# Kernel optimization log

Hardware: AMD Instinct MI355X
Metric: run time of the kernel (lower is better)

## Reference

```python
import jax, jax.numpy as jnp
import numpy as np

FLOAT_MIN = -100000.0

def setup_inputs() -> dict:
    key = jax.random.key(0)
    ks = jax.random.split(key, 6)
    B, S, Q, K = 16, 8192, 1024, 256
    stdv = 1.0 / np.sqrt(K)
    return {
        "query": jax.random.normal(ks[0], (B, Q), dtype=jnp.float32),
        "keys": jax.random.normal(ks[1], (B, S, K), dtype=jnp.float32),
        "values": jax.random.normal(ks[2], (B, S, K), dtype=jnp.float32),
        "kv_mask": jnp.ones((B, S, 1), dtype=jnp.float32),
        "W_attr": jax.random.uniform(ks[3], (K, Q), jnp.float32, -stdv, stdv),
        "b_attr": jax.random.uniform(ks[4], (K,), jnp.float32, -stdv, stdv),
        "V_attr": jax.random.uniform(ks[5], (K,), jnp.float32, -stdv, stdv),
    }

def reference(query, keys, values, kv_mask, W_attr, b_attr, V_attr):
    # projected query: [B, 1, K]
    q = jnp.einsum('bq,kq->bk', query, W_attr)[:, None, :]
    # additive energies: [B, S, 1]
    energies = jnp.einsum('bsk,k->bs', jnp.tanh(keys + q + b_attr), V_attr)[:, :, None]
    energies = kv_mask * energies + (1.0 - kv_mask) * FLOAT_MIN
    scores = jax.nn.softmax(energies, axis=1)          # [B, S, 1]
    ctx = jnp.sum(values * scores, axis=1)             # [B, V_dim]
    return (scores, ctx)
```

## Files before the change

kernel.cpp:

```cpp
#include <hip/hip_runtime.h>
#include <math.h>

#define BB 16
#define SS 8192
#define KK 256
#define QQ 1024

static constexpr float C2L2E = 2.88539008177792681f;
static constexpr float FLOAT_MIN_V = -100000.0f;

__device__ __forceinline__ float wave_sum(float v) {
#pragma unroll
  for (int off = 32; off >= 1; off >>= 1) v += __shfl_xor(v, off, 64);
  return v;
}

__global__ __launch_bounds__(256) void qproj_kernel(
    const float* __restrict__ query, const float* __restrict__ W,
    const float* __restrict__ b_attr, float* __restrict__ qb2) {
  const int blk = blockIdx.x;
  const int b = blk >> 6;
  const int kg = blk & 63;
  const int lane = threadIdx.x & 63;
  const int w = threadIdx.x >> 6;
  const int k = kg * 4 + w;

  const float4* q4 = (const float4*)(query + (size_t)b * QQ);
  const float4* w4 = (const float4*)(W + (size_t)k * QQ);
  float acc = 0.f;
#pragma unroll
  for (int j = 0; j < 4; ++j) {
    const float4 qv = q4[j * 64 + lane];
    const float4 wv = w4[j * 64 + lane];
    acc = fmaf(wv.x, qv.x, acc);
    acc = fmaf(wv.y, qv.y, acc);
    acc = fmaf(wv.z, qv.z, acc);
    acc = fmaf(wv.w, qv.w, acc);
  }
  acc = wave_sum(acc);
  if (lane == 0) qb2[b * KK + k] = C2L2E * (acc + b_attr[k]);
}

#define EROWS 64
__global__ __launch_bounds__(256) void energy_kernel(
    const float* __restrict__ keys, const float* __restrict__ V_attr,
    const float* __restrict__ qb2, float* __restrict__ e) {
  const int blk = blockIdx.x;
  const int b = blk / (SS / EROWS);
  const int lane = threadIdx.x & 63;
  const int w = threadIdx.x >> 6;
  const int s0 = (blk % (SS / EROWS)) * EROWS + w * (EROWS / 4);

  const float4 v4 = ((const float4*)V_attr)[lane];
  const float sv = wave_sum(v4.x + v4.y + v4.z + v4.w);
  const float4 nv2 =
      make_float4(-2.f * v4.x, -2.f * v4.y, -2.f * v4.z, -2.f * v4.w);
  const float4 qb = ((const float4*)qb2)[b * (KK / 4) + lane];

  const float* rowbase = keys + (size_t)(b * SS + s0) * KK;
  float4 kv = ((const float4*)rowbase)[lane];
  for (int i = 0; i < EROWS / 4; ++i) {
    const float4 cur = kv;
    if (i < EROWS / 4 - 1)
      kv = ((const float4*)(rowbase + (size_t)(i + 1) * KK))[lane];
    float r0 = __builtin_amdgcn_rcpf(
        1.f + __builtin_amdgcn_exp2f(fmaf(cur.x, C2L2E, qb.x)));
    float r1 = __builtin_amdgcn_rcpf(
        1.f + __builtin_amdgcn_exp2f(fmaf(cur.y, C2L2E, qb.y)));
    float r2 = __builtin_amdgcn_rcpf(
        1.f + __builtin_amdgcn_exp2f(fmaf(cur.z, C2L2E, qb.z)));
    float r3 = __builtin_amdgcn_rcpf(
        1.f + __builtin_amdgcn_exp2f(fmaf(cur.w, C2L2E, qb.w)));
    float p = fmaf(nv2.x, r0,
                   fmaf(nv2.y, r1, fmaf(nv2.z, r2, nv2.w * r3)));
    p = wave_sum(p);
    if (lane == 0) e[b * SS + s0 + i] = p + sv;
  }
}

__global__ __launch_bounds__(1024) void softmax_kernel(
    const float* __restrict__ e, const float* __restrict__ mask,
    float* __restrict__ scores) {
  const int b = blockIdx.x;
  const int tid = threadIdx.x;
  const int lane = tid & 63;
  const int wid = tid >> 6;
  __shared__ float red[16];

  float ev[8];
  float m = -3.4e38f;
#pragma unroll
  for (int i = 0; i < 8; ++i) {
    const int s = tid + i * 1024;
    const float mk = mask[b * SS + s];
    float x = e[b * SS + s];
    x = mk * x + (1.f - mk) * FLOAT_MIN_V;
    ev[i] = x;
    m = fmaxf(m, x);
  }
#pragma unroll
  for (int off = 32; off >= 1; off >>= 1) m = fmaxf(m, __shfl_xor(m, off, 64));
  if (lane == 0) red[wid] = m;
  __syncthreads();
  if (wid == 0) {
    float t = red[lane & 15];
#pragma unroll
    for (int off = 8; off >= 1; off >>= 1) t = fmaxf(t, __shfl_xor(t, off, 64));
    if (lane == 0) red[0] = t;
  }
  __syncthreads();
  m = red[0];
  __syncthreads();

  float pv[8];
  float l = 0.f;
#pragma unroll
  for (int i = 0; i < 8; ++i) {
    pv[i] = __expf(ev[i] - m);
    l += pv[i];
  }
  l = wave_sum(l);
  if (lane == 0) red[wid] = l;
  __syncthreads();
  if (wid == 0) {
    float t = red[lane & 15];
#pragma unroll
    for (int off = 8; off >= 1; off >>= 1) t += __shfl_xor(t, off, 64);
    if (lane == 0) red[0] = t;
  }
  __syncthreads();
  const float inv = 1.f / red[0];
#pragma unroll
  for (int i = 0; i < 8; ++i) scores[b * SS + tid + i * 1024] = pv[i] * inv;
}

#define CROWS 64
__global__ __launch_bounds__(256) void ctx_partial_kernel(
    const float* __restrict__ values, const float* __restrict__ scores,
    float* __restrict__ part) {
  const int blk = blockIdx.x;
  const int b = blk / (SS / CROWS);
  const int lane = threadIdx.x & 63;
  const int w = threadIdx.x >> 6;
  const int s0 = (blk % (SS / CROWS)) * CROWS + w * (CROWS / 4);

  const float* rowbase = values + (size_t)(b * SS + s0) * KK;
  float4 kv = ((const float4*)rowbase)[lane];
  float4 acc = make_float4(0.f, 0.f, 0.f, 0.f);
  for (int i = 0; i < CROWS / 4; ++i) {
    const float4 cur = kv;
    if (i < CROWS / 4 - 1)
      kv = ((const float4*)(rowbase + (size_t)(i + 1) * KK))[lane];
    const float p = scores[b * SS + s0 + i];
    acc.x = fmaf(p, cur.x, acc.x);
    acc.y = fmaf(p, cur.y, acc.y);
    acc.z = fmaf(p, cur.z, acc.z);
    acc.w = fmaf(p, cur.w, acc.w);
  }

  __shared__ float cacc[4][KK];
  ((float4*)&cacc[w][0])[lane] = acc;
  __syncthreads();
  const int t = threadIdx.x;
  part[(size_t)blk * KK + t] =
      cacc[0][t] + cacc[1][t] + cacc[2][t] + cacc[3][t];
}

__global__ __launch_bounds__(256) void ctx_reduce_kernel(
    const float* __restrict__ part, float* __restrict__ ctx) {
  const int b = blockIdx.x;
  const int t = threadIdx.x;
  const float* p = part + (size_t)b * (SS / CROWS) * KK + t;
  float s = 0.f;
#pragma unroll 8
  for (int j = 0; j < SS / CROWS; ++j) s += p[(size_t)j * KK];
  ctx[b * KK + t] = s;
}

extern "C" void kernel_launch(void* const* d_in, const int* in_sizes, int n_in,
                              void* d_out, int out_size, void* d_ws,
                              size_t ws_size, hipStream_t stream) {
  const float* query = (const float*)d_in[0];
  const float* keys = (const float*)d_in[1];
  const float* values = (const float*)d_in[2];
  const float* mask = (const float*)d_in[3];
  const float* W = (const float*)d_in[4];
  const float* b_attr = (const float*)d_in[5];
  const float* V_attr = (const float*)d_in[6];

  float* scores = (float*)d_out;
  float* ctx = scores + BB * SS;

  float* qb2 = (float*)d_ws;
  float* e = qb2 + BB * KK;
  float* part = e + BB * SS;

  qproj_kernel<<<BB * (KK / 4), 256, 0, stream>>>(query, W, b_attr, qb2);
  energy_kernel<<<BB * (SS / EROWS), 256, 0, stream>>>(keys, V_attr, qb2, e);
  softmax_kernel<<<BB, 1024, 0, stream>>>(e, mask, scores);
  ctx_partial_kernel<<<BB * (SS / CROWS), 256, 0, stream>>>(values, scores,
                                                            part);
  ctx_reduce_kernel<<<BB, 256, 0, stream>>>(part, ctx);
}
```

Baseline: 299.7 us.

## Fuse energy, softmax and context into one online-softmax split-K pass

Energy computation, masking and the context accumulation now run in one kernel. Each wave streams keys and values rows together and keeps a running max and sum (online softmax), and each block writes a partial max, sum and weighted accumulator. A finalize kernel merges the partials, normalises ctx and recomputes scores from the stored energies. This drops the separate softmax and ctx launches and the dependency between them. It adds non-temporal loads and some extra exp work per row.

```diff
diff --git a/kernel.cpp b/kernel.cpp
--- a/kernel.cpp
+++ b/kernel.cpp
@@ -7,12 +7,25 @@
 #define QQ 1024
 
 static constexpr float C2L2E = 2.88539008177792681f;
+static constexpr float L2E = 1.44269504088896341f;
 static constexpr float FLOAT_MIN_V = -100000.0f;
+
+typedef float floatx4 __attribute__((ext_vector_type(4)));
 
 __device__ __forceinline__ float wave_sum(float v) {
 #pragma unroll
   for (int off = 32; off >= 1; off >>= 1) v += __shfl_xor(v, off, 64);
   return v;
+}
+
+__device__ __forceinline__ float wave_max(float v) {
+#pragma unroll
+  for (int off = 32; off >= 1; off >>= 1) v = fmaxf(v, __shfl_xor(v, off, 64));
+  return v;
+}
+
+__device__ __forceinline__ floatx4 ldnt(const float* p) {
+  return __builtin_nontemporal_load((const floatx4*)p);
 }
 
 __global__ __launch_bounds__(256) void qproj_kernel(
@@ -41,15 +54,18 @@
   if (lane == 0) qb2[b * KK + k] = C2L2E * (acc + b_attr[k]);
 }
 
-#define EROWS 64
-__global__ __launch_bounds__(256) void energy_kernel(
-    const float* __restrict__ keys, const float* __restrict__ V_attr,
-    const float* __restrict__ qb2, float* __restrict__ e) {
+#define FROWS 64
+__global__ __launch_bounds__(256) void fused_kernel(
+    const float* __restrict__ keys, const float* __restrict__ values,
+    const float* __restrict__ mask, const float* __restrict__ V_attr,
+    const float* __restrict__ qb2, float* __restrict__ e,
+    float* __restrict__ part_m, float* __restrict__ part_l,
+    float* __restrict__ part_acc) {
   const int blk = blockIdx.x;
-  const int b = blk / (SS / EROWS);
+  const int b = blk / (SS / FROWS);
   const int lane = threadIdx.x & 63;
   const int w = threadIdx.x >> 6;
-  const int s0 = (blk % (SS / EROWS)) * EROWS + w * (EROWS / 4);
+  const int s0 = (blk % (SS / FROWS)) * FROWS + w * (FROWS / 4);
 
   const float4 v4 = ((const float4*)V_attr)[lane];
   const float sv = wave_sum(v4.x + v4.y + v4.z + v4.w);
@@ -57,124 +73,111 @@
       make_float4(-2.f * v4.x, -2.f * v4.y, -2.f * v4.z, -2.f * v4.w);
   const float4 qb = ((const float4*)qb2)[b * (KK / 4) + lane];
 
-  const float* rowbase = keys + (size_t)(b * SS + s0) * KK;
-  float4 kv = ((const float4*)rowbase)[lane];
-  for (int i = 0; i < EROWS / 4; ++i) {
-    const float4 cur = kv;
-    if (i < EROWS / 4 - 1)
-      kv = ((const float4*)(rowbase + (size_t)(i + 1) * KK))[lane];
+  const float* krow = keys + (size_t)(b * SS + s0) * KK;
+  const float* vrow = values + (size_t)(b * SS + s0) * KK;
+  floatx4 kf = ldnt(krow + 4 * lane);
+  floatx4 vf = ldnt(vrow + 4 * lane);
+
+  float m = -3.4e38f, l = 0.f;
+  float4 acc = make_float4(0.f, 0.f, 0.f, 0.f);
+  for (int i = 0; i < FROWS / 4; ++i) {
+    const floatx4 ck = kf;
+    const floatx4 cv = vf;
+    if (i < FROWS / 4 - 1) {
+      kf = ldnt(krow + (size_t)(i + 1) * KK + 4 * lane);
+      vf = ldnt(vrow + (size_t)(i + 1) * KK + 4 * lane);
+    }
+    const float mk = mask[b * SS + s0 + i];
     float r0 = __builtin_amdgcn_rcpf(
-        1.f + __builtin_amdgcn_exp2f(fmaf(cur.x, C2L2E, qb.x)));
+        1.f + __builtin_amdgcn_exp2f(fmaf(ck.x, C2L2E, qb.x)));
     float r1 = __builtin_amdgcn_rcpf(
-        1.f + __builtin_amdgcn_exp2f(fmaf(cur.y, C2L2E, qb.y)));
+        1.f + __builtin_amdgcn_exp2f(fmaf(ck.y, C2L2E, qb.y)));
     float r2 = __builtin_amdgcn_rcpf(
-        1.f + __builtin_amdgcn_exp2f(fmaf(cur.z, C2L2E, qb.z)));
+        1.f + __builtin_amdgcn_exp2f(fmaf(ck.z, C2L2E, qb.z)));
     float r3 = __builtin_amdgcn_rcpf(
-        1.f + __builtin_amdgcn_exp2f(fmaf(cur.w, C2L2E, qb.w)));
-    float p = fmaf(nv2.x, r0,
-                   fmaf(nv2.y, r1, fmaf(nv2.z, r2, nv2.w * r3)));
+        1.f + __builtin_amdgcn_exp2f(fmaf(ck.w, C2L2E, qb.w)));
+    float p = fmaf(nv2.x, r0, fmaf(nv2.y, r1, fmaf(nv2.z, r2, nv2.w * r3)));
     p = wave_sum(p);
-    if (lane == 0) e[b * SS + s0 + i] = p + sv;
-  }
-}
-
-__global__ __launch_bounds__(1024) void softmax_kernel(
-    const float* __restrict__ e, const float* __restrict__ mask,
-    float* __restrict__ scores) {
+    const float es = p + sv;
+    const float x = mk * es + (1.f - mk) * FLOAT_MIN_V;
+    if (lane == 0) e[b * SS + s0 + i] = x;
+    const float newm = fmaxf(m, x);
+    const float sc = __builtin_amdgcn_exp2f((m - newm) * L2E);
+    const float pe = __builtin_amdgcn_exp2f((x - newm) * L2E);
+    l = fmaf(l, sc, pe);
+    acc.x = fmaf(acc.x, sc, pe * cv.x);
+    acc.y = fmaf(acc.y, sc, pe * cv.y);
+    acc.z = fmaf(acc.z, sc, pe * cv.z);
+    acc.w = fmaf(acc.w, sc, pe * cv.w);
+    m = newm;
+  }
+
+  __shared__ float lacc[4][KK];
+  __shared__ float lm[4], ll[4];
+  ((float4*)&lacc[w][0])[lane] = acc;
+  if (lane == 0) {
+    lm[w] = m;
+    ll[w] = l;
+  }
+  __syncthreads();
+  const float M = fmaxf(fmaxf(lm[0], lm[1]), fmaxf(lm[2], lm[3]));
+  const float w0 = __builtin_amdgcn_exp2f((lm[0] - M) * L2E);
+  const float w1 = __builtin_amdgcn_exp2f((lm[1] - M) * L2E);
+  const float w2 = __builtin_amdgcn_exp2f((lm[2] - M) * L2E);
+  const float w3 = __builtin_amdgcn_exp2f((lm[3] - M) * L2E);
+  const int t = threadIdx.x;
+  const float ca =
+      fmaf(w0, lacc[0][t], fmaf(w1, lacc[1][t], fmaf(w2, lacc[2][t], w3 * lacc[3][t])));
+  part_acc[(size_t)blk * KK + t] = ca;
+  if (t == 0) {
+    part_m[blk] = M;
+    part_l[blk] = fmaf(w0, ll[0], fmaf(w1, ll[1], fmaf(w2, ll[2], w3 * ll[3])));
+  }
+}
+
+__global__ __launch_bounds__(1024) void finalize_kernel(
+    const float* __restrict__ part_m, const float* __restrict__ part_l,
+    const float* __restrict__ part_acc, const float* __restrict__ e,
+    float* __restrict__ scores, float* __restrict__ ctx) {
   const int b = blockIdx.x;
   const int tid = threadIdx.x;
   const int lane = tid & 63;
-  const int wid = tid >> 6;
-  __shared__ float red[16];
-
-  float ev[8];
-  float m = -3.4e38f;
-#pragma unroll
-  for (int i = 0; i < 8; ++i) {
-    const int s = tid + i * 1024;
-    const float mk = mask[b * SS + s];
-    float x = e[b * SS + s];
-    x = mk * x + (1.f - mk) * FLOAT_MIN_V;
-    ev[i] = x;
-    m = fmaxf(m, x);
-  }
-#pragma unroll
-  for (int off = 32; off >= 1; off >>= 1) m = fmaxf(m, __shfl_xor(m, off, 64));
-  if (lane == 0) red[wid] = m;
-  __syncthreads();
-  if (wid == 0) {
-    float t = red[lane & 15];
-#pragma unroll
-    for (int off = 8; off >= 1; off >>= 1) t = fmaxf(t, __shfl_xor(t, off, 64));
-    if (lane == 0) red[0] = t;
-  }
-  __syncthreads();
-  m = red[0];
-  __syncthreads();
-
-  float pv[8];
-  float l = 0.f;
-#pragma unroll
-  for (int i = 0; i < 8; ++i) {
-    pv[i] = __expf(ev[i] - m);
-    l += pv[i];
-  }
-  l = wave_sum(l);
-  if (lane == 0) red[wid] = l;
-  __syncthreads();
-  if (wid == 0) {
-    float t = red[lane & 15];
-#pragma unroll
-    for (int off = 8; off >= 1; off >>= 1) t += __shfl_xor(t, off, 64);
-    if (lane == 0) red[0] = t;
-  }
-  __syncthreads();
-  const float inv = 1.f / red[0];
-#pragma unroll
-  for (int i = 0; i < 8; ++i) scores[b * SS + tid + i * 1024] = pv[i] * inv;
-}
-
-#define CROWS 64
-__global__ __launch_bounds__(256) void ctx_partial_kernel(
-    const float* __restrict__ values, const float* __restrict__ scores,
-    float* __restrict__ part) {
-  const int blk = blockIdx.x;
-  const int b = blk / (SS / CROWS);
-  const int lane = threadIdx.x & 63;
-  const int w = threadIdx.x >> 6;
-  const int s0 = (blk % (SS / CROWS)) * CROWS + w * (CROWS / 4);
-
-  const float* rowbase = values + (size_t)(b * SS + s0) * KK;
-  float4 kv = ((const float4*)rowbase)[lane];
-  float4 acc = make_float4(0.f, 0.f, 0.f, 0.f);
-  for (int i = 0; i < CROWS / 4; ++i) {
-    const float4 cur = kv;
-    if (i < CROWS / 4 - 1)
-      kv = ((const float4*)(rowbase + (size_t)(i + 1) * KK))[lane];
-    const float p = scores[b * SS + s0 + i];
-    acc.x = fmaf(p, cur.x, acc.x);
-    acc.y = fmaf(p, cur.y, acc.y);
-    acc.z = fmaf(p, cur.z, acc.z);
-    acc.w = fmaf(p, cur.w, acc.w);
-  }
-
-  __shared__ float cacc[4][KK];
-  ((float4*)&cacc[w][0])[lane] = acc;
-  __syncthreads();
-  const int t = threadIdx.x;
-  part[(size_t)blk * KK + t] =
-      cacc[0][t] + cacc[1][t] + cacc[2][t] + cacc[3][t];
-}
-
-__global__ __launch_bounds__(256) void ctx_reduce_kernel(
-    const float* __restrict__ part, float* __restrict__ ctx) {
-  const int b = blockIdx.x;
-  const int t = threadIdx.x;
-  const float* p = part + (size_t)b * (SS / CROWS) * KK + t;
+  constexpr int NP = SS / FROWS;
+  __shared__ float sm[NP], sl[NP], sscale[NP];
+  __shared__ float cred[4][KK];
+
+  if (tid < NP) {
+    sm[tid] = part_m[b * NP + tid];
+    sl[tid] = part_l[b * NP + tid];
+  }
+  __syncthreads();
+
+  const float M = wave_max(fmaxf(sm[lane], sm[lane + 64]));
+  const float L = wave_sum(
+      fmaf(__builtin_amdgcn_exp2f((sm[lane] - M) * L2E), sl[lane],
+           __builtin_amdgcn_exp2f((sm[lane + 64] - M) * L2E) * sl[lane + 64]));
+  if (tid < NP) sscale[tid] = __builtin_amdgcn_exp2f((sm[tid] - M) * L2E);
+  __syncthreads();
+
+  const int g = tid >> 8;
+  const int k = tid & 255;
   float s = 0.f;
 #pragma unroll 8
-  for (int j = 0; j < SS / CROWS; ++j) s += p[(size_t)j * KK];
-  ctx[b * KK + t] = s;
+  for (int j = g * 32; j < g * 32 + 32; ++j)
+    s = fmaf(sscale[j], part_acc[(size_t)(b * NP + j) * KK + k], s);
+  cred[g][k] = s;
+  __syncthreads();
+  const float invL = 1.f / L;
+  if (tid < KK)
+    ctx[b * KK + tid] =
+        (cred[0][tid] + cred[1][tid] + cred[2][tid] + cred[3][tid]) * invL;
+
+#pragma unroll
+  for (int i = 0; i < 8; ++i) {
+    const int s_idx = tid + i * 1024;
+    const float x = e[b * SS + s_idx];
+    scores[b * SS + s_idx] = __builtin_amdgcn_exp2f((x - M) * L2E) * invL;
+  }
 }
 
 extern "C" void kernel_launch(void* const* d_in, const int* in_sizes, int n_in,
@@ -193,12 +196,13 @@
 
   float* qb2 = (float*)d_ws;
   float* e = qb2 + BB * KK;
-  float* part = e + BB * SS;
+  float* part_m = e + BB * SS;
+  float* part_l = part_m + BB * (SS / FROWS);
+  float* part_acc = part_l + BB * (SS / FROWS);
 
   qproj_kernel<<<BB * (KK / 4), 256, 0, stream>>>(query, W, b_attr, qb2);
-  energy_kernel<<<BB * (SS / EROWS), 256, 0, stream>>>(keys, V_attr, qb2, e);
-  softmax_kernel<<<BB, 1024, 0, stream>>>(e, mask, scores);
-  ctx_partial_kernel<<<BB * (SS / CROWS), 256, 0, stream>>>(values, scores,
-                                                            part);
-  ctx_reduce_kernel<<<BB, 256, 0, stream>>>(part, ctx);
-}
+  fused_kernel<<<BB * (SS / FROWS), 256, 0, stream>>>(
+      keys, values, mask, V_attr, qb2, e, part_m, part_l, part_acc);
+  finalize_kernel<<<BB, 1024, 0, stream>>>(part_m, part_l, part_acc, e,
+                                           scores, ctx);
+}
```

Result: faster. 276.1 us (-7.9%).
